# Optimization experiments

Measured on AMD Instinct MI355X. Metric: run time of the kernel, lower is better.

Reference implementation:

```python
import jax, jax.numpy as jnp
import numpy as np
import math

B, L, S, T = 16, 128, 128, 128
QDIM, FDIM, HID, ODIM = 512, 512, 512, 512

def setup_inputs() -> dict:
    key = jax.random.key(0)
    ks = jax.random.split(key, 9)
    sc = 0.02
    return {
        "query": jax.random.normal(ks[0], (B, L, QDIM), dtype=jnp.float32),
        "src": jax.random.normal(ks[1], (B, S, FDIM), dtype=jnp.float32),
        "trg": jax.random.normal(ks[2], (B, T, FDIM), dtype=jnp.float32),
        "Wq": jax.random.normal(ks[3], (QDIM, HID), dtype=jnp.float32) * sc,
        "bq": jnp.zeros((HID,), dtype=jnp.float32),
        "Ws": jax.random.normal(ks[4], (FDIM, HID), dtype=jnp.float32) * sc,
        "bs": jnp.zeros((HID,), dtype=jnp.float32),
        "Wo": jax.random.normal(ks[5], (FDIM * 2 + QDIM, ODIM), dtype=jnp.float32) * sc,
        "bo": jnp.zeros((ODIM,), dtype=jnp.float32),
    }

def reference(query, src, trg, Wq, bq, Ws, bs, Wo, bo):
    b, l, _ = query.shape
    s = src.shape[1]
    t = trg.shape[1]
    q = query @ Wq + bq            # [b,l,h]
    s_key = src @ Ws + bs          # [b,s,h]  (src_linear == trg_linear, shared weights)
    t_key = trg @ Ws + bs          # [b,t,h]
    # trilinear scores: [b,l,s,t]
    weight = jnp.einsum('blk,bsk,btk->blst', q, s_key, t_key) / math.sqrt(HID)
    weight = jax.nn.softmax(weight.reshape(b, l, s * t), axis=-1).reshape(b, l, s, t)
    s_ctx = jnp.einsum('blst,bsf->blf', weight, src)
    t_ctx = jnp.einsum('blst,btf->blf', weight, trg)
    x = jnp.concatenate((query, s_ctx, t_ctx), axis=-1)
    return x @ Wo + bo
```

## Files before the change

### kernel.cpp

```cpp
#include <hip/hip_runtime.h>
#include <hip/hip_bf16.h>

typedef __attribute__((ext_vector_type(8))) short short8;
typedef __attribute__((ext_vector_type(4))) short short4v;
typedef __attribute__((ext_vector_type(4))) float f32x4;
typedef __attribute__((ext_vector_type(8))) _Float16 half8;

#define DEVINL static __device__ __forceinline__

constexpr float SCORE_SCALE = 0.063758977414048896f;

typedef const __attribute__((address_space(1))) void gv_t;
typedef __attribute__((address_space(3))) void lv_t;
DEVINL void gload16(const void* g, void* l) {
  __builtin_amdgcn_global_load_lds((gv_t*)g, (lv_t*)l, 16, 0, 0);
}

#define SWZ_ADD(v, pat)                                                    \
  v += __int_as_float(__builtin_amdgcn_ds_swizzle(__float_as_int(v), pat))

template <int M>
DEVINL void gemm16(const _Float16* A, const _Float16* B, int K, int lda, int ldb,
                   _Float16* ldsA, _Float16* ldsB, f32x4 acc[M / 32][4])
{
  const int tid = threadIdx.x, lane = tid & 63;
  const int wr = (tid >> 7) & 1, wc = (tid >> 6) & 1;
  constexpr int NA = M / 32;
  int aoff[NA], boff[4];
#pragma unroll
  for (int i = 0; i < NA; ++i) {
    const int ci = tid + i * 256, row = ci >> 3, c = ci & 7;
    aoff[i] = row * lda + ((c ^ (row & 7)) << 3);
  }
#pragma unroll
  for (int i = 0; i < 4; ++i) {
    const int ci = tid + i * 256, row = ci >> 3, c = ci & 7;
    boff[i] = row * ldb + ((c ^ (row & 7)) << 3);
  }
#define G16STAGE(cur, kk)                                                        \
  {                                                                              \
    _Pragma("unroll")                                                            \
    for (int i = 0; i < NA; ++i)                                                 \
      gload16(A + aoff[i] + (kk), ldsA + (cur) * (M * 64) + (tid + i * 256) * 8);\
    _Pragma("unroll")                                                            \
    for (int i = 0; i < 4; ++i)                                                  \
      gload16(B + boff[i] + (kk), ldsB + (cur) * 8192 + (tid + i * 256) * 8);    \
  }
  G16STAGE(0, 0);
  __syncthreads();
  for (int kk = 0; kk < K; kk += 64) {
    const int cur = (kk >> 6) & 1;
    if (kk + 64 < K) G16STAGE(cur ^ 1, kk + 64);
    const _Float16* bA = ldsA + cur * (M * 64);
    const _Float16* bB = ldsB + cur * 8192;
#pragma unroll
    for (int s = 0; s < 2; ++s) {
      const int cg2 = s * 4 + (lane >> 4);
      half8 afr[NA], bfr[4];
#pragma unroll
      for (int mi = 0; mi < NA; ++mi) {
        const int r = wr * (M / 2) + mi * 16 + (lane & 15);
        afr[mi] = *(const half8*)(bA + r * 64 + ((cg2 ^ (r & 7)) << 3));
      }
#pragma unroll
      for (int ni = 0; ni < 4; ++ni) {
        const int r = wc * 64 + ni * 16 + (lane & 15);
        bfr[ni] = *(const half8*)(bB + r * 64 + ((cg2 ^ (r & 7)) << 3));
      }
#pragma unroll
      for (int mi = 0; mi < NA; ++mi)
#pragma unroll
        for (int ni = 0; ni < 4; ++ni)
          acc[mi][ni] = __builtin_amdgcn_mfma_f32_16x16x32_f16(afr[mi], bfr[ni], acc[mi][ni], 0, 0, 0);
    }
    __syncthreads();
  }
#undef G16STAGE
}

__global__ __launch_bounds__(256) void k_prep(
    const float* __restrict__ query, const float* __restrict__ src,
    const float* __restrict__ trg,
    const float* __restrict__ Wq, const float* __restrict__ Ws,
    const float* __restrict__ Wo,
    _Float16* __restrict__ x, _Float16* __restrict__ srch,
    _Float16* __restrict__ trgh,
    _Float16* __restrict__ WqT, _Float16* __restrict__ WsT,
    _Float16* __restrict__ WoT,
    _Float16* __restrict__ srcT, _Float16* __restrict__ trgT)
{
  __shared__ float t[32][33];
  const int id = blockIdx.x, tid = threadIdx.x;
  if (id < 1536) {
    const int z = id >> 9;
    const int idx8 = (((id & 511) << 8) + tid) * 8;
    const float* in = (z == 0) ? query : (z == 1) ? src : trg;
    float4 va = *(const float4*)(in + idx8);
    float4 vb = *(const float4*)(in + idx8 + 4);
    half8 h;
    h[0] = (_Float16)va.x; h[1] = (_Float16)va.y;
    h[2] = (_Float16)va.z; h[3] = (_Float16)va.w;
    h[4] = (_Float16)vb.x; h[5] = (_Float16)vb.y;
    h[6] = (_Float16)vb.z; h[7] = (_Float16)vb.w;
    if (z == 0) {
      const int row = idx8 >> 9, col = idx8 & 511;
      *(half8*)(x + (size_t)row * 1536 + col) = h;
    } else {
      _Float16* o = (z == 1) ? srch : trgh;
      *(half8*)(o + idx8) = h;
    }
    return;
  }
  const float* in; _Float16* out; int KK, NN, bx, by; size_t bo = 0;
  if (id < 1792)      { const int u = id - 1536; in = Wq;  out = WqT;  KK = 512;  NN = 512; bx = u & 15; by = u >> 4; }
  else if (id < 2048) { const int u = id - 1792; in = Ws;  out = WsT;  KK = 512;  NN = 512; bx = u & 15; by = u >> 4; }
  else if (id < 2816) { const int u = id - 2048; in = Wo;  out = WoT;  KK = 1536; NN = 512; bx = u & 15; by = u >> 4; }
  else if (id < 3840) { const int u = id - 2816; in = src; out = srcT; KK = 128;  NN = 512; bx = u & 15; by = (u >> 4) & 3; bo = (size_t)(u >> 6) * 65536; }
  else                { const int u = id - 3840; in = trg; out = trgT; KK = 128;  NN = 512; bx = u & 15; by = (u >> 4) & 3; bo = (size_t)(u >> 6) * 65536; }
  const int tx = tid & 31, ty = tid >> 5;
  const int k0 = by * 32, n0 = bx * 32;
#pragma unroll
  for (int i = 0; i < 4; ++i)
    t[ty + i * 8][tx] = in[bo + (size_t)(k0 + ty + i * 8) * NN + n0 + tx];
  __syncthreads();
#pragma unroll
  for (int i = 0; i < 4; ++i)
    out[bo + (size_t)(n0 + ty + i * 8) * KK + k0 + tx] = (_Float16)t[tx][ty + i * 8];
}

__global__ __launch_bounds__(256) void k_proj(
    const _Float16* __restrict__ xq, const _Float16* __restrict__ srch,
    const _Float16* __restrict__ trgh,
    const _Float16* __restrict__ WqT, const _Float16* __restrict__ WsT,
    const float* __restrict__ bq, const float* __restrict__ bs,
    _Float16* __restrict__ qh, _Float16* __restrict__ skh,
    _Float16* __restrict__ tkh)
{
  __shared__ __align__(16) _Float16 lds[32768];
  const int z = blockIdx.z;
  const _Float16* A = (z == 0) ? xq : (z == 1) ? srch : trgh;
  const int lda = (z == 0) ? 1536 : 512;
  const _Float16* BT = (z == 0) ? WqT : WsT;
  const float* bias = (z == 0) ? bq : bs;
  const int brow = blockIdx.y * 128, bcol = blockIdx.x * 128;

  f32x4 acc[4][4] = {};
  gemm16<128>(A + (size_t)brow * lda, BT + (size_t)bcol * 512, 512, lda, 512,
              lds, lds + 16384, acc);

  const int tid = threadIdx.x, lane = tid & 63;
  const int wr = (tid >> 7) & 1, wc = (tid >> 6) & 1;
  const int r0 = wr * 64 + ((lane >> 4) << 2);
  const int c0 = wc * 64 + (lane & 15);
#pragma unroll
  for (int mi = 0; mi < 4; ++mi)
#pragma unroll
    for (int ni = 0; ni < 4; ++ni) {
      const int col = bcol + c0 + ni * 16;
      const float bv = bias[col];
#pragma unroll
      for (int r = 0; r < 4; ++r) {
        const int row = brow + r0 + mi * 16 + r;
        const float v = acc[mi][ni][r] + bv;
        if (z == 0)      qh[(size_t)row * 512 + col] = (_Float16)(v * SCORE_SCALE);
        else if (z == 1) skh[(size_t)row * 512 + col] = (_Float16)v;
        else             tkh[(size_t)row * 512 + col] = (_Float16)v;
      }
    }
}

__global__ __launch_bounds__(512, 4) void k_score(
    const _Float16* __restrict__ qh, const _Float16* __restrict__ skh,
    const _Float16* __restrict__ tkh,
    _Float16* __restrict__ wct)
{
  __shared__ __align__(16) char pool[67584];
  _Float16* qlds = (_Float16*)(pool + 65536);
  float* wsp   = (float*)(pool);
  float* wtp   = (float*)(pool + 4096);
  float* wfin  = (float*)(pool + 8192);
  float* denom = (float*)(pool + 12288);

  const int raw = blockIdx.x;
  const int swz = (raw & 7) * 128 + (raw >> 3);
  const int b = swz >> 6, l0 = (swz & 63) * 2;

  const int tid = threadIdx.x, lane = tid & 63, wid = tid >> 6;
  const int l = wid >> 2, qs = (wid >> 1) & 1, qt = wid & 1;
  const int cg = lane >> 4;
  const _Float16* skb = skh + (size_t)b * 65536;
  const _Float16* tkb = tkh + (size_t)b * 65536;

  int soff[2];
#pragma unroll
  for (int j = 0; j < 2; ++j) {
    const int ci = j * 512 + tid;
    const int row = ci >> 3, c = ci & 7;
    soff[j] = row * 512 + ((c ^ (row & 7)) << 3);
  }

  if (tid < 256) {
    const int li = tid >> 7, e = (tid & 127) * 4;
    *(short4v*)(qlds + li * 512 + e) =
        *(const short4v*)(qh + (size_t)(b * 128 + l0 + li) * 512 + e);
  }

  const int rbase_s = (qs * 64 + (lane & 15)) * 128;
  const int rbase_t = (qt * 64 + (lane & 15)) * 128;
  const int sw0 = ((0 * 4 + cg) ^ (lane & 7)) << 4;
  const int sw1 = ((1 * 4 + cg) ^ (lane & 7)) << 4;

#define KSTAGE(dst, kk)                                                     \
  {                                                                         \
    char* base_ = pool + (dst) * 32768;                                     \
    _Pragma("unroll")                                                       \
    for (int j = 0; j < 2; ++j) {                                           \
      gload16(skb + soff[j] + (kk), base_ + (j * 512 + tid) * 16);          \
      gload16(tkb + soff[j] + (kk), base_ + 16384 + (j * 512 + tid) * 16);  \
    }                                                                       \
  }

  f32x4 acc[4][4] = {};
  KSTAGE(0, 0);
  __syncthreads();
  int buf = 0;
  for (int it = 0; it < 8; ++it) {
    if (it < 7) KSTAGE(buf ^ 1, (it + 1) * 64);
    const char* S = pool + buf * 32768;
    const char* T = S + 16384;
    const int kk = it * 64;
#pragma unroll
    for (int s = 0; s < 2; ++s) {
      const int swv = s ? sw1 : sw0;
      half8 qv = *(const half8*)(qlds + l * 512 + kk + s * 32 + cg * 8);
      half8 sfr[4], tfr[4];
#pragma unroll
      for (int mi = 0; mi < 4; ++mi)
        sfr[mi] = *(const half8*)(S + rbase_s + mi * 2048 + swv);
#pragma unroll
      for (int ni = 0; ni < 4; ++ni)
        tfr[ni] = *(const half8*)(T + rbase_t + ni * 2048 + swv);
      __builtin_amdgcn_s_setprio(1);
#pragma unroll
      for (int mi = 0; mi < 4; ++mi) {
        half8 a = sfr[mi] * qv;
#pragma unroll
        for (int ni = 0; ni < 4; ++ni)
          acc[mi][ni] = __builtin_amdgcn_mfma_f32_16x16x32_f16(a, tfr[ni], acc[mi][ni], 0, 0, 0);
      }
      __builtin_amdgcn_s_setprio(0);
    }
    __syncthreads();
    buf ^= 1;
  }
#undef KSTAGE

#pragma unroll
  for (int mi = 0; mi < 4; ++mi)
#pragma unroll
    for (int ni = 0; ni < 4; ++ni)
#pragma unroll
      for (int r = 0; r < 4; ++r)
        acc[mi][ni][r] = exp2f(acc[mi][ni][r]);

#pragma unroll
  for (int mi = 0; mi < 4; ++mi)
#pragma unroll
    for (int r = 0; r < 4; ++r) {
      float v = acc[mi][0][r] + acc[mi][1][r] + acc[mi][2][r] + acc[mi][3][r];
      SWZ_ADD(v, 0x041F);
      SWZ_ADD(v, 0x081F);
      SWZ_ADD(v, 0x101F);
      SWZ_ADD(v, 0x201F);
      if ((lane & 15) == 0)
        wsp[(l * 2 + qt) * 128 + qs * 64 + mi * 16 + (lane >> 4) * 4 + r] = v;
    }
#pragma unroll
  for (int ni = 0; ni < 4; ++ni) {
    float v = 0.f;
#pragma unroll
    for (int mi = 0; mi < 4; ++mi)
#pragma unroll
      for (int r = 0; r < 4; ++r) v += acc[mi][ni][r];
    SWZ_ADD(v, 0x401F);
    v += __shfl_xor(v, 32);
    if (lane < 16) wtp[(l * 2 + qs) * 128 + qt * 64 + ni * 16 + lane] = v;
  }
  __syncthreads();

  if (tid < 256) {
    const int li = tid >> 7, idx = tid & 127;
    wfin[(li * 2 + 0) * 128 + idx] =
        wsp[(li * 2 + 0) * 128 + idx] + wsp[(li * 2 + 1) * 128 + idx];
  } else {
    const int u = tid - 256, li = u >> 7, idx = u & 127;
    wfin[(li * 2 + 1) * 128 + idx] =
        wtp[(li * 2 + 0) * 128 + idx] + wtp[(li * 2 + 1) * 128 + idx];
  }
  __syncthreads();
  if (wid < 2) {
    float v = wfin[wid * 256 + lane] + wfin[wid * 256 + lane + 64];
#pragma unroll
    for (int off = 32; off >= 1; off >>= 1) v += __shfl_xor(v, off);
    if (lane == 0) denom[wid] = v;
  }
  __syncthreads();
  const float inv0 = 1.0f / denom[0], inv1 = 1.0f / denom[1];

  if (tid < 256) {
    const int li = tid >> 7, idx = tid & 127;
    const float inv = li ? inv1 : inv0;
    wct[((size_t)(b * 2 + 0) * 128 + l0 + li) * 128 + idx] =
        (_Float16)(wfin[li * 256 + idx] * inv);
  } else {
    const int u = tid - 256, li = u >> 7, idx = u & 127;
    const float inv = li ? inv1 : inv0;
    wct[((size_t)(b * 2 + 1) * 128 + l0 + li) * 128 + idx] =
        (_Float16)(wfin[li * 256 + 128 + idx] * inv);
  }
}

__global__ __launch_bounds__(256) void k_ctx(const _Float16* __restrict__ wct,
                                             const _Float16* __restrict__ srcT,
                                             const _Float16* __restrict__ trgT,
                                             _Float16* __restrict__ x)
{
  __shared__ __align__(16) _Float16 lds[32768];
  const int side = blockIdx.x, fcol = blockIdx.y, b = blockIdx.z;
  const _Float16* A  = wct + (size_t)(b * 2 + side) * 16384;
  const _Float16* BT = (side ? trgT : srcT) + (size_t)b * 65536 + fcol * 16384;

  f32x4 acc[4][4] = {};
  gemm16<128>(A, BT, 128, 128, 128, lds, lds + 16384, acc);

  const int tid = threadIdx.x, lane = tid & 63;
  const int wr = (tid >> 7) & 1, wc = (tid >> 6) & 1;
  const int r0 = wr * 64 + ((lane >> 4) << 2);
  const int c0 = wc * 64 + (lane & 15);
  const int xoff = 512 + side * 512 + fcol * 128;
#pragma unroll
  for (int mi = 0; mi < 4; ++mi)
#pragma unroll
    for (int ni = 0; ni < 4; ++ni) {
      const int col = c0 + ni * 16;
#pragma unroll
      for (int r = 0; r < 4; ++r) {
        const int row = r0 + mi * 16 + r;
        x[(size_t)(b * 128 + row) * 1536 + xoff + col] = (_Float16)acc[mi][ni][r];
      }
    }
}

__global__ __launch_bounds__(256) void k_out(const _Float16* __restrict__ x,
                                             const _Float16* __restrict__ WoT,
                                             const float* __restrict__ bo,
                                             float* __restrict__ out)
{
  __shared__ __align__(16) _Float16 lds[24576];
  const int brow = blockIdx.y * 64, bcol = blockIdx.x * 128;
  f32x4 acc[2][4] = {};
  gemm16<64>(x + (size_t)brow * 1536, WoT + (size_t)bcol * 1536, 1536, 1536, 1536,
             lds, lds + 8192, acc);
  const int tid = threadIdx.x, lane = tid & 63;
  const int wr = (tid >> 7) & 1, wc = (tid >> 6) & 1;
  const int r0 = wr * 32 + ((lane >> 4) << 2);
  const int c0 = wc * 64 + (lane & 15);
#pragma unroll
  for (int mi = 0; mi < 2; ++mi)
#pragma unroll
    for (int ni = 0; ni < 4; ++ni) {
      const int col = bcol + c0 + ni * 16;
      const float bv = bo[col];
#pragma unroll
      for (int r = 0; r < 4; ++r) {
        const int row = brow + r0 + mi * 16 + r;
        out[(size_t)row * 512 + col] = acc[mi][ni][r] + bv;
      }
    }
}

extern "C" void kernel_launch(void* const* d_in, const int* in_sizes, int n_in,
                              void* d_out, int out_size, void* d_ws, size_t ws_size,
                              hipStream_t stream)
{
  (void)in_sizes; (void)n_in; (void)out_size; (void)ws_size;
  const float* query = (const float*)d_in[0];
  const float* src   = (const float*)d_in[1];
  const float* trg   = (const float*)d_in[2];
  const float* Wq    = (const float*)d_in[3];
  const float* bq    = (const float*)d_in[4];
  const float* Ws    = (const float*)d_in[5];
  const float* bs    = (const float*)d_in[6];
  const float* Wo    = (const float*)d_in[7];
  const float* bo    = (const float*)d_in[8];
  float* out = (float*)d_out;

  char* w = (char*)d_ws;
  _Float16* x    = (_Float16*)(w);
  _Float16* qh   = (_Float16*)(w + (6u  << 20));
  _Float16* skh  = (_Float16*)(w + (8u  << 20));
  _Float16* tkh  = (_Float16*)(w + (10u << 20));
  _Float16* srch = (_Float16*)(w + (12u << 20));
  _Float16* trgh = (_Float16*)(w + (14u << 20));
  _Float16* WqT  = (_Float16*)(w + (16u << 20));
  _Float16* WsT  = (_Float16*)(w + (16u << 20) + 512 * 512 * 2);
  _Float16* WoT  = (_Float16*)(w + (17u << 20));
  _Float16* srcT = (_Float16*)(w + (19u << 20));
  _Float16* trgT = (_Float16*)(w + (21u << 20));
  _Float16* wct  = (_Float16*)(w + (23u << 20));

  k_prep<<<4864, 256, 0, stream>>>(query, src, trg, Wq, Ws, Wo,
                                   x, srch, trgh, WqT, WsT, WoT, srcT, trgT);
  k_proj<<<dim3(4, 16, 3), 256, 0, stream>>>(x, srch, trgh, WqT, WsT, bq, bs, qh, skh, tkh);
  k_score<<<1024, 512, 0, stream>>>(qh, skh, tkh, wct);
  k_ctx<<<dim3(2, 4, 16), 256, 0, stream>>>(wct, srcT, trgT, x);
  k_out<<<dim3(4, 32), 256, 0, stream>>>(x, WoT, bo, out);
}
```

Baseline: 82.27 us.

## Use 32x32 MFMA in score kernel and shrink GEMM tiles for more blocks

The score kernel moves from 16x16x32 MFMA tiles to 32x32x16 MFMA with f32x16 accumulators, which cuts the number of LDS fragment loads per MFMA. Its row-sum and column-sum reductions are rewritten to match the new accumulator layout. The shared GEMM helper gains a separate N tile parameter, and proj, ctx and out use smaller tiles (64x128 or 64x64) with larger grids to fill more CUs. Smaller tiles give less data reuse per block, and the new reduction index math is a correctness risk.

Result: slower. 88.87 us (+8.0%).

```diff
diff --git a/kernel.cpp b/kernel.cpp
--- a/kernel.cpp
+++ b/kernel.cpp
@@ -4,6 +4,7 @@
 typedef __attribute__((ext_vector_type(8))) short short8;
 typedef __attribute__((ext_vector_type(4))) short short4v;
 typedef __attribute__((ext_vector_type(4))) float f32x4;
+typedef __attribute__((ext_vector_type(16))) float f32x16;
 typedef __attribute__((ext_vector_type(8))) _Float16 half8;
 
 #define DEVINL static __device__ __forceinline__
@@ -19,32 +20,32 @@
 #define SWZ_ADD(v, pat)                                                    \
   v += __int_as_float(__builtin_amdgcn_ds_swizzle(__float_as_int(v), pat))
 
-template <int M>
+template <int M, int N>
 DEVINL void gemm16(const _Float16* A, const _Float16* B, int K, int lda, int ldb,
-                   _Float16* ldsA, _Float16* ldsB, f32x4 acc[M / 32][4])
+                   _Float16* ldsA, _Float16* ldsB, f32x4 acc[M / 32][N / 32])
 {
   const int tid = threadIdx.x, lane = tid & 63;
   const int wr = (tid >> 7) & 1, wc = (tid >> 6) & 1;
-  constexpr int NA = M / 32;
-  int aoff[NA], boff[4];
-#pragma unroll
-  for (int i = 0; i < NA; ++i) {
+  constexpr int MA = M / 32, NB = N / 32;
+  int aoff[MA], boff[NB];
+#pragma unroll
+  for (int i = 0; i < MA; ++i) {
     const int ci = tid + i * 256, row = ci >> 3, c = ci & 7;
     aoff[i] = row * lda + ((c ^ (row & 7)) << 3);
   }
 #pragma unroll
-  for (int i = 0; i < 4; ++i) {
+  for (int i = 0; i < NB; ++i) {
     const int ci = tid + i * 256, row = ci >> 3, c = ci & 7;
     boff[i] = row * ldb + ((c ^ (row & 7)) << 3);
   }
 #define G16STAGE(cur, kk)                                                        \
   {                                                                              \
     _Pragma("unroll")                                                            \
-    for (int i = 0; i < NA; ++i)                                                 \
+    for (int i = 0; i < MA; ++i)                                                 \
       gload16(A + aoff[i] + (kk), ldsA + (cur) * (M * 64) + (tid + i * 256) * 8);\
     _Pragma("unroll")                                                            \
-    for (int i = 0; i < 4; ++i)                                                  \
-      gload16(B + boff[i] + (kk), ldsB + (cur) * 8192 + (tid + i * 256) * 8);    \
+    for (int i = 0; i < NB; ++i)                                                 \
+      gload16(B + boff[i] + (kk), ldsB + (cur) * (N * 64) + (tid + i * 256) * 8);\
   }
   G16STAGE(0, 0);
   __syncthreads();
@@ -52,25 +53,25 @@
     const int cur = (kk >> 6) & 1;
     if (kk + 64 < K) G16STAGE(cur ^ 1, kk + 64);
     const _Float16* bA = ldsA + cur * (M * 64);
-    const _Float16* bB = ldsB + cur * 8192;
+    const _Float16* bB = ldsB + cur * (N * 64);
 #pragma unroll
     for (int s = 0; s < 2; ++s) {
       const int cg2 = s * 4 + (lane >> 4);
-      half8 afr[NA], bfr[4];
-#pragma unroll
-      for (int mi = 0; mi < NA; ++mi) {
+      half8 afr[MA], bfr[NB];
+#pragma unroll
+      for (int mi = 0; mi < MA; ++mi) {
         const int r = wr * (M / 2) + mi * 16 + (lane & 15);
         afr[mi] = *(const half8*)(bA + r * 64 + ((cg2 ^ (r & 7)) << 3));
       }
 #pragma unroll
-      for (int ni = 0; ni < 4; ++ni) {
-        const int r = wc * 64 + ni * 16 + (lane & 15);
+      for (int ni = 0; ni < NB; ++ni) {
+        const int r = wc * (N / 2) + ni * 16 + (lane & 15);
         bfr[ni] = *(const half8*)(bB + r * 64 + ((cg2 ^ (r & 7)) << 3));
       }
 #pragma unroll
-      for (int mi = 0; mi < NA; ++mi)
-#pragma unroll
-        for (int ni = 0; ni < 4; ++ni)
+      for (int mi = 0; mi < MA; ++mi)
+#pragma unroll
+        for (int ni = 0; ni < NB; ++ni)
           acc[mi][ni] = __builtin_amdgcn_mfma_f32_16x16x32_f16(afr[mi], bfr[ni], acc[mi][ni], 0, 0, 0);
     }
     __syncthreads();
@@ -136,24 +137,24 @@
     _Float16* __restrict__ qh, _Float16* __restrict__ skh,
     _Float16* __restrict__ tkh)
 {
-  __shared__ __align__(16) _Float16 lds[32768];
+  __shared__ __align__(16) _Float16 lds[24576];
   const int z = blockIdx.z;
   const _Float16* A = (z == 0) ? xq : (z == 1) ? srch : trgh;
   const int lda = (z == 0) ? 1536 : 512;
   const _Float16* BT = (z == 0) ? WqT : WsT;
   const float* bias = (z == 0) ? bq : bs;
-  const int brow = blockIdx.y * 128, bcol = blockIdx.x * 128;
-
-  f32x4 acc[4][4] = {};
-  gemm16<128>(A + (size_t)brow * lda, BT + (size_t)bcol * 512, 512, lda, 512,
-              lds, lds + 16384, acc);
+  const int brow = blockIdx.y * 64, bcol = blockIdx.x * 128;
+
+  f32x4 acc[2][4] = {};
+  gemm16<64, 128>(A + (size_t)brow * lda, BT + (size_t)bcol * 512, 512, lda, 512,
+                  lds, lds + 8192, acc);
 
   const int tid = threadIdx.x, lane = tid & 63;
   const int wr = (tid >> 7) & 1, wc = (tid >> 6) & 1;
-  const int r0 = wr * 64 + ((lane >> 4) << 2);
+  const int r0 = wr * 32 + ((lane >> 4) << 2);
   const int c0 = wc * 64 + (lane & 15);
 #pragma unroll
-  for (int mi = 0; mi < 4; ++mi)
+  for (int mi = 0; mi < 2; ++mi)
 #pragma unroll
     for (int ni = 0; ni < 4; ++ni) {
       const int col = bcol + c0 + ni * 16;
@@ -187,7 +188,8 @@
 
   const int tid = threadIdx.x, lane = tid & 63, wid = tid >> 6;
   const int l = wid >> 2, qs = (wid >> 1) & 1, qt = wid & 1;
-  const int cg = lane >> 4;
+  const int h = lane >> 5;
+  const int lr = lane & 31;
   const _Float16* skb = skh + (size_t)b * 65536;
   const _Float16* tkb = tkh + (size_t)b * 65536;
 
@@ -205,10 +207,9 @@
         *(const short4v*)(qh + (size_t)(b * 128 + l0 + li) * 512 + e);
   }
 
-  const int rbase_s = (qs * 64 + (lane & 15)) * 128;
-  const int rbase_t = (qt * 64 + (lane & 15)) * 128;
-  const int sw0 = ((0 * 4 + cg) ^ (lane & 7)) << 4;
-  const int sw1 = ((1 * 4 + cg) ^ (lane & 7)) << 4;
+  const int rs0 = (qs * 64 + lr) * 128;
+  const int rt0 = (qt * 64 + lr) * 128;
+  const int r7 = lr & 7;
 
 #define KSTAGE(dst, kk)                                                     \
   {                                                                         \
@@ -220,7 +221,7 @@
     }                                                                       \
   }
 
-  f32x4 acc[4][4] = {};
+  f32x16 acc[2][2] = {};
   KSTAGE(0, 0);
   __syncthreads();
   int buf = 0;
@@ -228,26 +229,21 @@
     if (it < 7) KSTAGE(buf ^ 1, (it + 1) * 64);
     const char* S = pool + buf * 32768;
     const char* T = S + 16384;
-    const int kk = it * 64;
-#pragma unroll
-    for (int s = 0; s < 2; ++s) {
-      const int swv = s ? sw1 : sw0;
-      half8 qv = *(const half8*)(qlds + l * 512 + kk + s * 32 + cg * 8);
-      half8 sfr[4], tfr[4];
-#pragma unroll
-      for (int mi = 0; mi < 4; ++mi)
-        sfr[mi] = *(const half8*)(S + rbase_s + mi * 2048 + swv);
-#pragma unroll
-      for (int ni = 0; ni < 4; ++ni)
-        tfr[ni] = *(const half8*)(T + rbase_t + ni * 2048 + swv);
+#pragma unroll
+    for (int ci = 0; ci < 4; ++ci) {
+      const int sw = ((2 * ci + h) ^ r7) << 4;
+      half8 qv = *(const half8*)(qlds + l * 512 + it * 64 + ci * 16 + h * 8);
+      half8 s0 = *(const half8*)(S + rs0 + sw);
+      half8 s1 = *(const half8*)(S + rs0 + 4096 + sw);
+      half8 t0 = *(const half8*)(T + rt0 + sw);
+      half8 t1 = *(const half8*)(T + rt0 + 4096 + sw);
+      half8 a0 = s0 * qv;
+      half8 a1 = s1 * qv;
       __builtin_amdgcn_s_setprio(1);
-#pragma unroll
-      for (int mi = 0; mi < 4; ++mi) {
-        half8 a = sfr[mi] * qv;
-#pragma unroll
-        for (int ni = 0; ni < 4; ++ni)
-          acc[mi][ni] = __builtin_amdgcn_mfma_f32_16x16x32_f16(a, tfr[ni], acc[mi][ni], 0, 0, 0);
-      }
+      acc[0][0] = __builtin_amdgcn_mfma_f32_32x32x16_f16(a0, t0, acc[0][0], 0, 0, 0);
+      acc[0][1] = __builtin_amdgcn_mfma_f32_32x32x16_f16(a0, t1, acc[0][1], 0, 0, 0);
+      acc[1][0] = __builtin_amdgcn_mfma_f32_32x32x16_f16(a1, t0, acc[1][0], 0, 0, 0);
+      acc[1][1] = __builtin_amdgcn_mfma_f32_32x32x16_f16(a1, t1, acc[1][1], 0, 0, 0);
       __builtin_amdgcn_s_setprio(0);
     }
     __syncthreads();
@@ -256,35 +252,35 @@
 #undef KSTAGE
 
 #pragma unroll
-  for (int mi = 0; mi < 4; ++mi)
-#pragma unroll
-    for (int ni = 0; ni < 4; ++ni)
-#pragma unroll
-      for (int r = 0; r < 4; ++r)
+  for (int mi = 0; mi < 2; ++mi)
+#pragma unroll
+    for (int ni = 0; ni < 2; ++ni)
+#pragma unroll
+      for (int r = 0; r < 16; ++r)
         acc[mi][ni][r] = exp2f(acc[mi][ni][r]);
 
 #pragma unroll
-  for (int mi = 0; mi < 4; ++mi)
-#pragma unroll
-    for (int r = 0; r < 4; ++r) {
-      float v = acc[mi][0][r] + acc[mi][1][r] + acc[mi][2][r] + acc[mi][3][r];
+  for (int mi = 0; mi < 2; ++mi)
+#pragma unroll
+    for (int reg = 0; reg < 16; ++reg) {
+      float v = acc[mi][0][reg] + acc[mi][1][reg];
       SWZ_ADD(v, 0x041F);
       SWZ_ADD(v, 0x081F);
       SWZ_ADD(v, 0x101F);
       SWZ_ADD(v, 0x201F);
-      if ((lane & 15) == 0)
-        wsp[(l * 2 + qt) * 128 + qs * 64 + mi * 16 + (lane >> 4) * 4 + r] = v;
-    }
-#pragma unroll
-  for (int ni = 0; ni < 4; ++ni) {
+      SWZ_ADD(v, 0x401F);
+      if (lr == 0)
+        wsp[(l * 2 + qt) * 128 + qs * 64 + mi * 32 + (reg & 3) + 8 * (reg >> 2) + 4 * h] = v;
+    }
+#pragma unroll
+  for (int ni = 0; ni < 2; ++ni) {
     float v = 0.f;
 #pragma unroll
-    for (int mi = 0; mi < 4; ++mi)
-#pragma unroll
-      for (int r = 0; r < 4; ++r) v += acc[mi][ni][r];
-    SWZ_ADD(v, 0x401F);
+    for (int mi = 0; mi < 2; ++mi)
+#pragma unroll
+      for (int reg = 0; reg < 16; ++reg) v += acc[mi][ni][reg];
     v += __shfl_xor(v, 32);
-    if (lane < 16) wtp[(l * 2 + qs) * 128 + qt * 64 + ni * 16 + lane] = v;
+    if (lane < 32) wtp[(l * 2 + qs) * 128 + qt * 64 + ni * 32 + lr] = v;
   }
   __syncthreads();
 
@@ -325,27 +321,28 @@
                                              const _Float16* __restrict__ trgT,
                                              _Float16* __restrict__ x)
 {
-  __shared__ __align__(16) _Float16 lds[32768];
-  const int side = blockIdx.x, fcol = blockIdx.y, b = blockIdx.z;
-  const _Float16* A  = wct + (size_t)(b * 2 + side) * 16384;
+  __shared__ __align__(16) _Float16 lds[24576];
+  const int side = blockIdx.x, fcol = blockIdx.y >> 1, mrow = blockIdx.y & 1;
+  const int b = blockIdx.z;
+  const _Float16* A  = wct + (size_t)(b * 2 + side) * 16384 + mrow * 64 * 128;
   const _Float16* BT = (side ? trgT : srcT) + (size_t)b * 65536 + fcol * 16384;
 
-  f32x4 acc[4][4] = {};
-  gemm16<128>(A, BT, 128, 128, 128, lds, lds + 16384, acc);
+  f32x4 acc[2][4] = {};
+  gemm16<64, 128>(A, BT, 128, 128, 128, lds, lds + 8192, acc);
 
   const int tid = threadIdx.x, lane = tid & 63;
   const int wr = (tid >> 7) & 1, wc = (tid >> 6) & 1;
-  const int r0 = wr * 64 + ((lane >> 4) << 2);
+  const int r0 = wr * 32 + ((lane >> 4) << 2);
   const int c0 = wc * 64 + (lane & 15);
   const int xoff = 512 + side * 512 + fcol * 128;
 #pragma unroll
-  for (int mi = 0; mi < 4; ++mi)
+  for (int mi = 0; mi < 2; ++mi)
 #pragma unroll
     for (int ni = 0; ni < 4; ++ni) {
       const int col = c0 + ni * 16;
 #pragma unroll
       for (int r = 0; r < 4; ++r) {
-        const int row = r0 + mi * 16 + r;
+        const int row = mrow * 64 + r0 + mi * 16 + r;
         x[(size_t)(b * 128 + row) * 1536 + xoff + col] = (_Float16)acc[mi][ni][r];
       }
     }
@@ -356,19 +353,19 @@
                                              const float* __restrict__ bo,
                                              float* __restrict__ out)
 {
-  __shared__ __align__(16) _Float16 lds[24576];
-  const int brow = blockIdx.y * 64, bcol = blockIdx.x * 128;
-  f32x4 acc[2][4] = {};
-  gemm16<64>(x + (size_t)brow * 1536, WoT + (size_t)bcol * 1536, 1536, 1536, 1536,
-             lds, lds + 8192, acc);
+  __shared__ __align__(16) _Float16 lds[16384];
+  const int brow = blockIdx.y * 64, bcol = blockIdx.x * 64;
+  f32x4 acc[2][2] = {};
+  gemm16<64, 64>(x + (size_t)brow * 1536, WoT + (size_t)bcol * 1536, 1536, 1536, 1536,
+                 lds, lds + 8192, acc);
   const int tid = threadIdx.x, lane = tid & 63;
   const int wr = (tid >> 7) & 1, wc = (tid >> 6) & 1;
   const int r0 = wr * 32 + ((lane >> 4) << 2);
-  const int c0 = wc * 64 + (lane & 15);
+  const int c0 = wc * 32 + (lane & 15);
 #pragma unroll
   for (int mi = 0; mi < 2; ++mi)
 #pragma unroll
-    for (int ni = 0; ni < 4; ++ni) {
+    for (int ni = 0; ni < 2; ++ni) {
       const int col = bcol + c0 + ni * 16;
       const float bv = bo[col];
 #pragma unroll
@@ -411,8 +408,8 @@
 
   k_prep<<<4864, 256, 0, stream>>>(query, src, trg, Wq, Ws, Wo,
                                    x, srch, trgh, WqT, WsT, WoT, srcT, trgT);
-  k_proj<<<dim3(4, 16, 3), 256, 0, stream>>>(x, srch, trgh, WqT, WsT, bq, bs, qh, skh, tkh);
+  k_proj<<<dim3(4, 32, 3), 256, 0, stream>>>(x, srch, trgh, WqT, WsT, bq, bs, qh, skh, tkh);
   k_score<<<1024, 512, 0, stream>>>(qh, skh, tkh, wct);
-  k_ctx<<<dim3(2, 4, 16), 256, 0, stream>>>(wct, srcT, trgT, x);
-  k_out<<<dim3(4, 32), 256, 0, stream>>>(x, WoT, bo, out);
-}
+  k_ctx<<<dim3(2, 8, 16), 256, 0, stream>>>(wct, srcT, trgT, x);
+  k_out<<<dim3(8, 32), 256, 0, stream>>>(x, WoT, bo, out);
+}
```
